# Kernel optimization log

Hardware: AMD Instinct MI355X
Metric: run time of the kernel (lower is better)

The kernel has to match this reference:

```python
import jax, jax.numpy as jnp
import numpy as np


def setup_inputs() -> dict:
    key = jax.random.key(0)
    ks = jax.random.split(key, 8)
    B, Cin, H, W = 4, 256, 64, 64
    Ck = Cin // 2            # 128, KAN in/out dim
    NC = 21                  # num_classes
    return {
        "x": jax.random.normal(ks[0], (B, Cin, H, W), dtype=jnp.float32),
        "conv1_w": jax.random.normal(ks[1], (Ck, Cin, 3, 3), dtype=jnp.float32) * 0.02,
        "conv1_b": jnp.zeros((Ck,), dtype=jnp.float32),
        "kan_scale": jnp.ones((Ck, Ck), dtype=jnp.float32)
                     + 0.1 * jax.random.normal(ks[2], (Ck, Ck), dtype=jnp.float32),
        "kan_translation": 0.1 * jax.random.normal(ks[3], (Ck, Ck), dtype=jnp.float32),
        "kan_wavelet_weight": jax.random.normal(ks[4], (Ck, Ck), dtype=jnp.float32) * 0.1,
        "kan_base_weight": jax.random.normal(ks[5], (Ck, Ck), dtype=jnp.float32) * 0.05,
        "conv2_w": jax.random.normal(ks[6], (NC, Ck, 1, 1), dtype=jnp.float32) * 0.05,
        "conv2_b": jnp.zeros((NC,), dtype=jnp.float32),
    }


def _conv2d(x, w, b, pad):
    y = jax.lax.conv_general_dilated(
        x, w, window_strides=(1, 1), padding=pad,
        dimension_numbers=("NCHW", "OIHW", "NCHW"))
    return y + b[None, :, None, None]


def _wavelet_kan(x, scale, translation, wav_w, base_w):
    # x: (N, Cin). Wav-KAN (DoG) layer:
    #   u = (x - translation) / scale, per (out, in) pair -> (N, O, I)
    #   dog(u) = -u * exp(-u^2 / 2)
    #   wavelet_out[n, o] = sum_i dog(u)[n, o, i] * wav_w[o, i]
    #   base_out = silu(x) @ base_w.T
    u = (x[:, None, :] - translation[None]) / scale[None]          # (N, O, I)
    dog = -u * jnp.exp(-0.5 * u * u)                               # (N, O, I)
    wav_out = jnp.einsum("noi,oi->no", dog, wav_w)                 # (N, O)
    base_out = jnp.einsum("ni,oi->no", jax.nn.silu(x), base_w)     # (N, O)
    return wav_out + base_out


def reference(x, conv1_w, conv1_b, kan_scale, kan_translation,
              kan_wavelet_weight, kan_base_weight, conv2_w, conv2_b):
    h = jax.nn.relu(_conv2d(x, conv1_w, conv1_b, ((1, 1), (1, 1))))   # (B, Ck, H, W)
    B, C, H, W = h.shape
    flat = h.transpose(0, 2, 3, 1).reshape(B * H * W, C)              # (N, Ck)
    k = _wavelet_kan(flat, kan_scale, kan_translation,
                     kan_wavelet_weight, kan_base_weight)             # (N, Ck)
    k = k.reshape(B, H, W, -1).transpose(0, 3, 1, 2)                  # (B, Ck, H, W)
    return _conv2d(k, conv2_w, conv2_b, ((0, 0), (0, 0)))             # (B, NC, H, W)
```

## Files before the change

kernel.cpp:

```cpp
#include <hip/hip_runtime.h>
#include <math.h>

typedef __attribute__((ext_vector_type(8))) short s16x8;
typedef __attribute__((ext_vector_type(4))) float f32x4;
typedef __attribute__((ext_vector_type(2))) float f32x2;

#define LOG2E 1.4426950408889634f

#define OFF_XH   0
#define OFF_WB   2097152
#define OFF_PQT  2244608
#define OFF_W2   2310144
#define OFF_H    2315520

__global__ __launch_bounds__(256) void prep_all_k(
    const float* __restrict__ x, const float* __restrict__ w1,
    const float* __restrict__ ks, const float* __restrict__ kt,
    const float* __restrict__ kw, const float* __restrict__ kb,
    const float* __restrict__ w2, float* __restrict__ ws) {
  int blk = blockIdx.x;
  int t = threadIdx.x;
  if (blk < 1024) {
    __shared__ float lsm[64][65];
    unsigned short* xh = (unsigned short*)(ws + OFF_XH);
    int pr = blk & 63, cib = (blk >> 6) & 3, bb = blk >> 8;
    int sp0 = pr * 64;
    const float* src = x + (unsigned)(bb * 256 + cib * 64) * 4096 + sp0;
#pragma unroll
    for (int rr = 0; rr < 16; ++rr) {
      int idx = rr * 256 + t;
      int ci = idx >> 6, px = idx & 63;
      lsm[ci][px] = src[ci * 4096 + px];
    }
    __syncthreads();
#pragma unroll
    for (int rr = 0; rr < 16; ++rr) {
      int idx = rr * 256 + t;
      int px = idx >> 6, ci = idx & 63;
      unsigned u = __float_as_uint(lsm[ci][px]);
      xh[(unsigned)(bb * 4096 + sp0 + px) * 256 + cib * 64 + ci] =
          (unsigned short)((u + 0x7FFF + ((u >> 16) & 1)) >> 16);
    }
  } else if (blk < 2251) {
    int tid = (blk - 1024) * 256 + t;
    unsigned short* Wb = (unsigned short*)(ws + OFF_WB);
    if (tid < 294912) {
      int j = tid & 7, co = (tid >> 3) & 63, g = (tid >> 9) & 3, r = tid >> 11;
      int t9 = r % 9, q = r / 9, ck = q & 7, chh = q >> 3;
      int ci = ck * 32 + g * 8 + j, cog = chh * 64 + co;
      unsigned u = __float_as_uint(w1[(unsigned)(cog * 256 + ci) * 9 + t9]);
      Wb[tid] = (unsigned short)((u + 0x7FFF + ((u >> 16) & 1)) >> 16);
    } else if (tid < 294912 + 16384) {
      int i2 = tid - 294912;
      int i = i2 >> 7, o = i2 & 127;
      int ic = i >> 3, k = i & 7;
      float rs = 1.f / ks[o * 128 + i];
      float T  = kt[o * 128 + i];
      float A  = -0.7213475204444817f * rs * rs;
      float Bq = -2.f * A * T;
      float C  = A * T * T;
      float P0 = -rs * kw[o * 128 + i];
      float sc = exp2f(C);
      int khi = k >> 2, klo = k & 3;
      unsigned base = ((unsigned)ic * 8 * 128 + o) * 4 + klo;
      ws[OFF_PQT + base + (0 + khi) * 512] = A;
      ws[OFF_PQT + base + (2 + khi) * 512] = Bq;
      ws[OFF_PQT + base + (4 + khi) * 512] = P0 * sc;
      ws[OFF_PQT + base + (6 + khi) * 512] = -P0 * T * sc;
    } else if (tid < 294912 + 16384 + 2688) {
      int i3 = tid - 294912 - 16384;
      int nc = i3 >> 7, k = i3 & 127;
      ws[OFF_W2 + nc * 256 + k] = w2[nc * 128 + k];
    }
  } else {
    int nc = blk - 2251;
    if (t < 128) {
      float acc = 0.f;
      for (int o = 0; o < 128; ++o)
        acc = fmaf(w2[nc * 128 + o], kb[o * 128 + t], acc);
      ws[OFF_W2 + nc * 256 + 128 + t] = acc;
    }
  }
}

__global__ __launch_bounds__(256, 2) void conv1_mfma_k(
    const unsigned short* __restrict__ xh, const unsigned short* __restrict__ Wb,
    const float* __restrict__ b1, float* __restrict__ h) {
  __shared__ unsigned short Asm[4 * 66 * 40];
  __shared__ unsigned short Bsm[18432];
  int blk = blockIdx.x;
  int ch = blk & 1, yt = (blk >> 1) & 31, bb = blk >> 6;
  int y0 = yt * 2;
  int t = threadIdx.x;
  int wave = t >> 6, lane = t & 63;
  int wn = wave & 1, wm = wave >> 1;
  int l15 = lane & 15, lg = lane >> 4;

  if (t < 8) {
    int r = t >> 1, xl = (t & 1) * 65;
    float4 z = {0, 0, 0, 0};
    float4* p = (float4*)&Asm[(r * 66 + xl) * 40];
    p[0] = z; p[1] = z; p[2] = z; p[3] = z; p[4] = z;
  }

  f32x4 acc[4][2];
  f32x4 zz = {0.f, 0.f, 0.f, 0.f};
#pragma unroll
  for (int f = 0; f < 4; ++f) { acc[f][0] = zz; acc[f][1] = zz; }

  int r_st = t >> 6, x_st = t & 63;
  int gy = y0 - 1 + r_st;
  bool yok = (gy >= 0) & (gy < 64);
  const unsigned short* asrc = xh + (unsigned)(bb * 4096 + gy * 64 + x_st) * 256;
  unsigned short* adst = &Asm[(r_st * 66 + x_st + 1) * 40];
  const unsigned short* bslab = Wb + ch * 8 * 18432;

  for (int ck = 0; ck < 8; ++ck) {
    float4 v0 = {0, 0, 0, 0}, v1 = v0, v2 = v0, v3 = v0;
    if (yok) {
      const float4* s = (const float4*)(asrc + ck * 32);
      v0 = s[0]; v1 = s[1]; v2 = s[2]; v3 = s[3];
    }
    { float4* d = (float4*)adst; d[0] = v0; d[1] = v1; d[2] = v2; d[3] = v3; }
    {
      const float4* s = (const float4*)(bslab + ck * 18432);
      float4* d = (float4*)Bsm;
#pragma unroll
      for (int j = 0; j < 9; ++j) d[j * 256 + t] = s[j * 256 + t];
    }
    __syncthreads();
#pragma unroll
    for (int t9 = 0; t9 < 9; ++t9) {
      int ky = t9 / 3, kx = t9 % 3;
      s16x8 a[4], b[2];
      int abase = ((wm + ky) * 66 + l15 + kx) * 40 + lg * 8;
#pragma unroll
      for (int f = 0; f < 4; ++f)
        a[f] = *(const s16x8*)&Asm[abase + f * 640];
#pragma unroll
      for (int n = 0; n < 2; ++n)
        b[n] = *(const s16x8*)&Bsm[((t9 * 4 + lg) * 64 + wn * 32 + n * 16 + l15) * 8];
#pragma unroll
      for (int f = 0; f < 4; ++f)
#pragma unroll
        for (int n = 0; n < 2; ++n)
          acc[f][n] = __builtin_amdgcn_mfma_f32_16x16x32_bf16(a[f], b[n], acc[f][n], 0, 0, 0);
    }
    __syncthreads();
  }
#pragma unroll
  for (int n = 0; n < 2; ++n) {
    int co = ch * 64 + wn * 32 + n * 16 + l15;
    float bz = b1[co];
#pragma unroll
    for (int f = 0; f < 4; ++f) {
      int xbase = f * 16 + lg * 4;
      float* dst = h + (unsigned)(bb * 4096 + (y0 + wm) * 64 + xbase) * 128 + co;
#pragma unroll
      for (int r = 0; r < 4; ++r) {
        float v = acc[f][n][r] + bz;
        dst[r * 128] = v > 0.f ? v : 0.f;
      }
    }
  }
}

__global__ __launch_bounds__(512) void wavkan_conv2_k(
    const float* __restrict__ h, const float* __restrict__ PQT,
    const float* __restrict__ w2c, const float* __restrict__ b2,
    float* __restrict__ out) {
  __shared__ float hsm[8][132];
  __shared__ float red[3][2][8][64];
  __shared__ float ksm[8][132];
  int n0 = blockIdx.x * 8;
  int t = threadIdx.x;
  if (t < 256) {
    int row = t >> 5, c4 = (t & 31) * 4;
    *(float4*)&hsm[row][c4] = *(const float4*)&h[(unsigned)(n0 + row) * 128 + c4];
  }
  __syncthreads();

  int wave = t >> 6, lane = t & 63;
  int ich = wave & 3;
  int oh  = wave >> 2;
  int o   = oh * 64 + lane;

  f32x2 accv[8];
#pragma unroll
  for (int n = 0; n < 8; ++n) accv[n] = (f32x2){0.f, 0.f};

  const float4* pq = (const float4*)PQT + o;

  for (int ic = ich * 4; ic < ich * 4 + 4; ++ic) {
    const float4* pp = pq + (unsigned)ic * 1024;
    float4 r0 = pp[0],   r1 = pp[128], r2 = pp[256], r3 = pp[384],
           r4 = pp[512], r5 = pp[640], r6 = pp[768], r7 = pp[896];
    f32x2 A2[4] = {{r0.x, r0.y}, {r0.z, r0.w}, {r1.x, r1.y}, {r1.z, r1.w}};
    f32x2 B2[4] = {{r2.x, r2.y}, {r2.z, r2.w}, {r3.x, r3.y}, {r3.z, r3.w}};
    f32x2 P2[4] = {{r4.x, r4.y}, {r4.z, r4.w}, {r5.x, r5.y}, {r5.z, r5.w}};
    f32x2 D2[4] = {{r6.x, r6.y}, {r6.z, r6.w}, {r7.x, r7.y}, {r7.z, r7.w}};
    int i0 = ic * 8;
#pragma unroll
    for (int n = 0; n < 8; ++n) {
      float4 h0 = *(const float4*)&hsm[n][i0];
      float4 h1 = *(const float4*)&hsm[n][i0 + 4];
      f32x2 hh[4] = {{h0.x, h0.y}, {h0.z, h0.w}, {h1.x, h1.y}, {h1.z, h1.w}};
      f32x2 a2 = accv[n];
#pragma unroll
      for (int q = 0; q < 4; ++q) {
        f32x2 h2 = hh[q];
        f32x2 t2 = A2[q] * h2 + B2[q];
        f32x2 u2 = t2 * h2;
        f32x2 e2;
        e2.x = __builtin_amdgcn_exp2f(u2.x);
        e2.y = __builtin_amdgcn_exp2f(u2.y);
        f32x2 v2 = P2[q] * h2 + D2[q];
        a2 = v2 * e2 + a2;
      }
      accv[n] = a2;
    }
  }

  if (ich) {
#pragma unroll
    for (int n = 0; n < 8; ++n)
      red[ich - 1][oh][n][lane] = accv[n].x + accv[n].y;
  }
  __syncthreads();
  if (!ich) {
#pragma unroll
    for (int n = 0; n < 8; ++n) {
      ksm[n][o] = (accv[n].x + accv[n].y) + red[0][oh][n][lane] +
                  red[1][oh][n][lane] + red[2][oh][n][lane];
    }
  }
  if (t < 256) {
    int n = t >> 5, c4 = (t & 31) * 4;
    float4 v = *(float4*)&hsm[n][c4];
    float4 s;
    s.x = v.x * __builtin_amdgcn_rcpf(1.f + __builtin_amdgcn_exp2f(-LOG2E * v.x));
    s.y = v.y * __builtin_amdgcn_rcpf(1.f + __builtin_amdgcn_exp2f(-LOG2E * v.y));
    s.z = v.z * __builtin_amdgcn_rcpf(1.f + __builtin_amdgcn_exp2f(-LOG2E * v.z));
    s.w = v.w * __builtin_amdgcn_rcpf(1.f + __builtin_amdgcn_exp2f(-LOG2E * v.w));
    *(float4*)&hsm[n][c4] = s;
  }
  __syncthreads();

  if (t < 168) {
    int n = t & 7, g = t >> 3;
    const float* w0 = w2c + g * 256;
    const float* kr = &ksm[n][0];
    const float* hr = &hsm[n][0];
    float a0 = 0.f;
#pragma unroll 4
    for (int k4 = 0; k4 < 32; ++k4) {
      float4 kv = *(const float4*)&kr[k4 * 4];
      float4 w = *(const float4*)&w0[k4 * 4];
      a0 += kv.x * w.x + kv.y * w.y + kv.z * w.z + kv.w * w.w;
    }
#pragma unroll 4
    for (int k4 = 0; k4 < 32; ++k4) {
      float4 hv = *(const float4*)&hr[k4 * 4];
      float4 w = *(const float4*)&w0[128 + k4 * 4];
      a0 += hv.x * w.x + hv.y * w.y + hv.z * w.z + hv.w * w.w;
    }
    int gn = n0 + n, bb = gn >> 12, sp = gn & 4095;
    out[(unsigned)(bb * 21 + g) * 4096 + sp] = a0 + b2[g];
  }
}

extern "C" void kernel_launch(void* const* d_in, const int* in_sizes, int n_in,
                              void* d_out, int out_size, void* d_ws, size_t ws_size,
                              hipStream_t stream) {
  const float* x  = (const float*)d_in[0];
  const float* w1 = (const float*)d_in[1];
  const float* b1 = (const float*)d_in[2];
  const float* ks = (const float*)d_in[3];
  const float* kt = (const float*)d_in[4];
  const float* kw = (const float*)d_in[5];
  const float* kb = (const float*)d_in[6];
  const float* w2 = (const float*)d_in[7];
  const float* b2 = (const float*)d_in[8];
  float* out = (float*)d_out;
  float* ws  = (float*)d_ws;

  prep_all_k<<<2272, 256, 0, stream>>>(x, w1, ks, kt, kw, kb, w2, ws);
  conv1_mfma_k<<<256, 256, 0, stream>>>((const unsigned short*)(ws + OFF_XH),
                                        (const unsigned short*)(ws + OFF_WB),
                                        b1, ws + OFF_H);
  wavkan_conv2_k<<<2048, 512, 0, stream>>>(ws + OFF_H, ws + OFF_PQT,
                                           ws + OFF_W2, b2, out);
}
```

Baseline: 82.60 us.

## Double-buffer conv1 LDS tiles and skip DoG math for zero activations

The conv1 MFMA kernel now double-buffers its A and B LDS tiles. The next channel chunk is prefetched into registers during the MFMA loop and stored to the other buffer afterwards, so only one barrier is needed per iteration. This doubles LDS use to roughly 115KB and drops the two-blocks-per-CU launch bound, which likely leaves one block per CU. Separately, the KAN inner loop checks whether a wave-uniform pair of ReLU outputs is zero. If so it adds only the constant term instead of evaluating exp2 and the FMAs, which exploits ReLU sparsity at the cost of a scalar branch per pair.

Result: slower. 156.6 us (+89.6%).

```diff
diff --git a/kernel.cpp b/kernel.cpp
--- a/kernel.cpp
+++ b/kernel.cpp
@@ -83,11 +83,11 @@
   }
 }
 
-__global__ __launch_bounds__(256, 2) void conv1_mfma_k(
+__global__ __launch_bounds__(256) void conv1_mfma_k(
     const unsigned short* __restrict__ xh, const unsigned short* __restrict__ Wb,
     const float* __restrict__ b1, float* __restrict__ h) {
-  __shared__ unsigned short Asm[4 * 66 * 40];
-  __shared__ unsigned short Bsm[18432];
+  __shared__ unsigned short Asm[2][4 * 66 * 40];
+  __shared__ unsigned short Bsm[2][18432];
   int blk = blockIdx.x;
   int ch = blk & 1, yt = (blk >> 1) & 31, bb = blk >> 6;
   int y0 = yt * 2;
@@ -96,10 +96,10 @@
   int wn = wave & 1, wm = wave >> 1;
   int l15 = lane & 15, lg = lane >> 4;
 
-  if (t < 8) {
-    int r = t >> 1, xl = (t & 1) * 65;
+  if (t < 16) {
+    int bf = t >> 3, r = (t >> 1) & 3, xl = (t & 1) * 65;
     float4 z = {0, 0, 0, 0};
-    float4* p = (float4*)&Asm[(r * 66 + xl) * 40];
+    float4* p = (float4*)&Asm[bf][(r * 66 + xl) * 40];
     p[0] = z; p[1] = z; p[2] = z; p[3] = z; p[4] = z;
   }
 
@@ -112,23 +112,43 @@
   int gy = y0 - 1 + r_st;
   bool yok = (gy >= 0) & (gy < 64);
   const unsigned short* asrc = xh + (unsigned)(bb * 4096 + gy * 64 + x_st) * 256;
-  unsigned short* adst = &Asm[(r_st * 66 + x_st + 1) * 40];
+  int aoff = (r_st * 66 + x_st + 1) * 40;
   const unsigned short* bslab = Wb + ch * 8 * 18432;
 
+  float4 av0 = {0,0,0,0}, av1 = av0, av2 = av0, av3 = av0;
+  float4 bv[9];
+  if (yok) {
+    const float4* s = (const float4*)(asrc);
+    av0 = s[0]; av1 = s[1]; av2 = s[2]; av3 = s[3];
+  }
+  {
+    const float4* s = (const float4*)(bslab);
+#pragma unroll
+    for (int j = 0; j < 9; ++j) bv[j] = s[j * 256 + t];
+  }
+  {
+    float4* d = (float4*)&Asm[0][aoff];
+    d[0] = av0; d[1] = av1; d[2] = av2; d[3] = av3;
+    float4* db = (float4*)&Bsm[0][0];
+#pragma unroll
+    for (int j = 0; j < 9; ++j) db[j * 256 + t] = bv[j];
+  }
+  __syncthreads();
+
   for (int ck = 0; ck < 8; ++ck) {
-    float4 v0 = {0, 0, 0, 0}, v1 = v0, v2 = v0, v3 = v0;
-    if (yok) {
-      const float4* s = (const float4*)(asrc + ck * 32);
-      v0 = s[0]; v1 = s[1]; v2 = s[2]; v3 = s[3];
-    }
-    { float4* d = (float4*)adst; d[0] = v0; d[1] = v1; d[2] = v2; d[3] = v3; }
-    {
-      const float4* s = (const float4*)(bslab + ck * 18432);
-      float4* d = (float4*)Bsm;
-#pragma unroll
-      for (int j = 0; j < 9; ++j) d[j * 256 + t] = s[j * 256 + t];
-    }
-    __syncthreads();
+    int cur = ck & 1;
+    if (ck < 7) {
+      av0 = (float4){0,0,0,0}; av1 = av0; av2 = av0; av3 = av0;
+      if (yok) {
+        const float4* s = (const float4*)(asrc + (ck + 1) * 32);
+        av0 = s[0]; av1 = s[1]; av2 = s[2]; av3 = s[3];
+      }
+      const float4* s = (const float4*)(bslab + (ck + 1) * 18432);
+#pragma unroll
+      for (int j = 0; j < 9; ++j) bv[j] = s[j * 256 + t];
+    }
+    const unsigned short* As = &Asm[cur][0];
+    const unsigned short* Bs = &Bsm[cur][0];
 #pragma unroll
     for (int t9 = 0; t9 < 9; ++t9) {
       int ky = t9 / 3, kx = t9 % 3;
@@ -136,15 +156,22 @@
       int abase = ((wm + ky) * 66 + l15 + kx) * 40 + lg * 8;
 #pragma unroll
       for (int f = 0; f < 4; ++f)
-        a[f] = *(const s16x8*)&Asm[abase + f * 640];
+        a[f] = *(const s16x8*)&As[abase + f * 640];
 #pragma unroll
       for (int n = 0; n < 2; ++n)
-        b[n] = *(const s16x8*)&Bsm[((t9 * 4 + lg) * 64 + wn * 32 + n * 16 + l15) * 8];
+        b[n] = *(const s16x8*)&Bs[((t9 * 4 + lg) * 64 + wn * 32 + n * 16 + l15) * 8];
 #pragma unroll
       for (int f = 0; f < 4; ++f)
 #pragma unroll
         for (int n = 0; n < 2; ++n)
           acc[f][n] = __builtin_amdgcn_mfma_f32_16x16x32_bf16(a[f], b[n], acc[f][n], 0, 0, 0);
+    }
+    if (ck < 7) {
+      float4* d = (float4*)&Asm[cur ^ 1][aoff];
+      d[0] = av0; d[1] = av1; d[2] = av2; d[3] = av3;
+      float4* db = (float4*)&Bsm[cur ^ 1][0];
+#pragma unroll
+      for (int j = 0; j < 9; ++j) db[j * 256 + t] = bv[j];
     }
     __syncthreads();
   }
@@ -209,13 +236,18 @@
 #pragma unroll
       for (int q = 0; q < 4; ++q) {
         f32x2 h2 = hh[q];
-        f32x2 t2 = A2[q] * h2 + B2[q];
-        f32x2 u2 = t2 * h2;
-        f32x2 e2;
-        e2.x = __builtin_amdgcn_exp2f(u2.x);
-        e2.y = __builtin_amdgcn_exp2f(u2.y);
-        f32x2 v2 = P2[q] * h2 + D2[q];
-        a2 = v2 * e2 + a2;
+        unsigned hz = __float_as_uint(h2.x) | __float_as_uint(h2.y);
+        if (__builtin_amdgcn_readfirstlane(hz) == 0) {
+          a2 = a2 + D2[q];
+        } else {
+          f32x2 t2 = A2[q] * h2 + B2[q];
+          f32x2 u2 = t2 * h2;
+          f32x2 e2;
+          e2.x = __builtin_amdgcn_exp2f(u2.x);
+          e2.y = __builtin_amdgcn_exp2f(u2.y);
+          f32x2 v2 = P2[q] * h2 + D2[q];
+          a2 = v2 * e2 + a2;
+        }
       }
       accv[n] = a2;
     }
```
